# Kernel tuning notes

Hardware: AMD Instinct MI355X
Metric: run time of the kernel (lower is better)

## Reference

```python
import jax, jax.numpy as jnp
import numpy as np

D_K = 24
ALPHA = 0.1
N_HEADS = 6
D_MODEL = 144
LN_EPS = 1e-5


def setup_inputs() -> dict:
    key = jax.random.key(0)
    ks = jax.random.split(key, 8)
    B, S = 8, 2048
    Q = jax.random.normal(ks[0], (B, S, D_MODEL), dtype=jnp.float32)
    K = jax.random.normal(ks[1], (B, N_HEADS, S, D_K), dtype=jnp.float32)
    V = jax.random.normal(ks[2], (B, N_HEADS, S, D_K), dtype=jnp.float32)
    attn_mask = jax.random.randint(ks[3], (B, S, S), 0, 2).astype(bool)
    Wq_w = jax.random.normal(ks[4], (D_MODEL, D_MODEL), dtype=jnp.float32) * 0.05
    Wq_b = jnp.zeros((D_MODEL,), dtype=jnp.float32)
    lin_w = jax.random.normal(ks[5], (D_MODEL, D_MODEL), dtype=jnp.float32) * 0.05
    lin_b = jnp.zeros((D_MODEL,), dtype=jnp.float32)
    ln_g = jnp.ones((D_MODEL,), dtype=jnp.float32)
    ln_b = jnp.zeros((D_MODEL,), dtype=jnp.float32)
    return {"Q": Q, "K": K, "V": V, "attn_mask": attn_mask,
            "Wq_w": Wq_w, "Wq_b": Wq_b, "lin_w": lin_w, "lin_b": lin_b,
            "ln_g": ln_g, "ln_b": ln_b}


def reference(Q, K, V, attn_mask, Wq_w, Wq_b, lin_w, lin_b, ln_g, ln_b):
    B, S, _ = Q.shape
    residual = Q
    # W_Q projection then head split: [B,S,D] -> [B,H,S,d_k]
    q = (Q @ Wq_w.T + Wq_b).reshape(B, S, N_HEADS, D_K).transpose(0, 2, 1, 3)
    # scores [B,H,S,Sk]; custom tanh activation instead of softmax
    scores = jnp.einsum('bhqd,bhkd->bhqk', q, K) / np.sqrt(D_K).astype(np.float32)
    attn = jnp.tanh(ALPHA * scores)
    # NOTE: original calls attn.masked_fill(...) non-inplace and drops the
    # result, so attn_mask has no effect. Faithfully ignored here.
    context = jnp.einsum('bhqk,bhkd->bhqd', attn, V)
    context = context.transpose(0, 2, 1, 3).reshape(B, S, N_HEADS * D_K)
    output = context @ lin_w.T + lin_b
    x = output + residual
    mu = jnp.mean(x, axis=-1, keepdims=True)
    var = jnp.var(x, axis=-1, keepdims=True)
    return (x - mu) / jnp.sqrt(var + LN_EPS) * ln_g + ln_b
```

## Files before the change

kernel.cpp:

```cpp
#include <hip/hip_runtime.h>
#include <hip/hip_bf16.h>

#define B_  8
#define S_  2048
#define H_  6
#define DK_ 24
#define DM_ 144

#define TK0  2.0412414523193153e-02f
#define TK1 -2.8350575726379381e-06f
#define TK2  4.7250959543965635e-10f

typedef __bf16 bf16x8 __attribute__((ext_vector_type(8)));
typedef __bf16 bf16x2 __attribute__((ext_vector_type(2)));
typedef float  f32x4  __attribute__((ext_vector_type(4)));
typedef float  f32x2  __attribute__((ext_vector_type(2)));

#define MFMA_ __builtin_amdgcn_mfma_f32_16x16x32_bf16

__device__ __forceinline__ unsigned short f2bf(float f) {
    return __builtin_bit_cast(unsigned short, (__bf16)f);
}
__device__ __forceinline__ uint pack2(float a, float b) {
    bf16x2 v; v[0] = (__bf16)a; v[1] = (__bf16)b;
    return __builtin_bit_cast(uint, v);
}
__device__ __forceinline__ uint tanh2_pack(float a, float b) {
    f32x2 c; c[0] = a; c[1] = b;
    f32x2 t = c * c;
    f32x2 u = t * TK2 + TK1;
    u = t * u + TK0;
    f32x2 r = c * u;
    return pack2(r[0], r[1]);
}

__device__ __forceinline__ void swap32(uint &x, uint &y) {
    auto r = __builtin_amdgcn_permlane32_swap(x, y, false, false);
    x = r[0]; y = r[1];
}
__device__ __forceinline__ void swap16(uint &x, uint &y, bool hi16) {
#if __has_builtin(__builtin_amdgcn_permlane16_swap)
    (void)hi16;
    auto r = __builtin_amdgcn_permlane16_swap(x, y, false, false);
    x = r[0]; y = r[1];
#else
    uint xs = __builtin_amdgcn_ds_swizzle(x, 0x401F);
    uint ys = __builtin_amdgcn_ds_swizzle(y, 0x401F);
    uint nx = hi16 ? ys : x;
    uint ny = hi16 ? y : xs;
    x = nx; y = ny;
#endif
}

__global__ __launch_bounds__(256)
void prep_kernel(const float* __restrict__ K, const float* __restrict__ V,
                 const float* __restrict__ Wq, const float* __restrict__ Wqb,
                 const float* __restrict__ Wl, const float* __restrict__ lb,
                 ushort* __restrict__ Ktt, ushort* __restrict__ Vtt,
                 ushort* __restrict__ Whq, ushort* __restrict__ Wlp) {
    __shared__ float sv[64 * 25];
    const int t = threadIdx.x;
    const int bid = blockIdx.x;
    if (bid >= 1536) {
        int i = (bid - 1536) * 256 + t;
        if (i < 30720) {
            int h = i / 5120, rem = i % 5120;
            int d = rem / 160, c = rem % 160;
            float v = 0.f;
            if (d < DK_) {
                if (c < DM_)       v = Wq[(h * DK_ + d) * DM_ + c];
                else if (c == DM_) v = Wqb[h * DK_ + d];
            }
            Whq[i] = f2bf(v);
        } else if (i < 53760) {
            int j = i - 30720;
            int r = j / 160, c = j % 160;
            float v = (c < DM_) ? Wl[r * DM_ + c] : (c == DM_ ? lb[r] : 0.f);
            Wlp[j] = f2bf(v);
        }
        return;
    }
    const int kt = bid & 31, h = (bid >> 5) % H_, b = bid / (32 * H_);
    const int bh = b * H_ + h;
    const size_t tile = (size_t)(bh * 32 + kt);
    const float4* Ks = (const float4*)(K + ((size_t)bh * S_ + kt * 64) * DK_);
    ushort* Ko = Ktt + tile * 2048;
    for (int idx = t; idx < 384; idx += 256) {
        int r = idx / 6, c4 = (idx % 6) * 4;
        float4 v = Ks[idx];
        ushort4 u; u.x = f2bf(v.x); u.y = f2bf(v.y); u.z = f2bf(v.z); u.w = f2bf(v.w);
        *(ushort4*)&Ko[r * 32 + c4] = u;
    }
    if (t < 64) { uint4 z = {0u,0u,0u,0u}; *(uint4*)&Ko[t * 32 + 24] = z; }
    const float4* Vs = (const float4*)(V + ((size_t)bh * S_ + kt * 64) * DK_);
    for (int idx = t; idx < 384; idx += 256) {
        int r = idx / 6, c4 = (idx % 6) * 4;
        *(float4*)&sv[r * 25 + c4] = Vs[idx];
    }
    __syncthreads();
    int d = t >> 3, s8 = (t & 7) * 8;
    uint4 o = {0u,0u,0u,0u};
    if (d < DK_) {
        o.x = pack2(sv[(s8 + 0) * 25 + d], sv[(s8 + 1) * 25 + d]);
        o.y = pack2(sv[(s8 + 2) * 25 + d], sv[(s8 + 3) * 25 + d]);
        o.z = pack2(sv[(s8 + 4) * 25 + d], sv[(s8 + 5) * 25 + d]);
        o.w = pack2(sv[(s8 + 6) * 25 + d], sv[(s8 + 7) * 25 + d]);
    }
    ((uint4*)Vtt)[tile * 256 + t] = o;
}

__global__ __launch_bounds__(512, 6)
void attn_kernel(const float* __restrict__ Q, const ushort* __restrict__ Whq,
                 const ushort* __restrict__ Ktt, const ushort* __restrict__ Vtt,
                 ushort* __restrict__ Cb) {
    __shared__ __attribute__((aligned(16))) char smem[38912];
    ushort* s_k  = (ushort*)smem;
    ushort* s_vt = (ushort*)(smem + 20480);
    ushort* s_q  = (ushort*)smem;
    float*  s_ctx = (float*)smem;

    const int t = threadIdx.x;
    const int w = t >> 6, n16 = t & 15, g = (t >> 4) & 3;
    const bool hi16 = (t & 16) != 0;
    const int qp = blockIdx.x, h = blockIdx.y, b = blockIdx.z;
    const int bh = b * H_ + h;
    const int row0 = qp * 128;

    const uint4* Kb4 = (const uint4*)Ktt + (size_t)bh * 8192;
    const uint4* Vb4 = (const uint4*)Vtt + (size_t)bh * 8192;

    const int t2 = t & 255;
    const bool isK = (t < 256);
    const int stoff = isK ? ((t2 >> 2) * 40 + (t2 & 3) * 8)
                          : ((t2 >> 3) * 72 + (t2 & 7) * 8);
    uint4 sreg0 = isK ? Kb4[t2] : Vb4[t2];
    uint4 sreg1 = isK ? Kb4[256 + t2] : Vb4[256 + t2];

    const f32x4 zf = {0.f, 0.f, 0.f, 0.f};
    const uint4* Wh4 = (const uint4*)Whq + h * 640;
    {
        const float* Qr = Q + (size_t)(b * S_ + row0 + w * 16 + n16) * DM_;
        f32x4 qa0 = zf, qa1 = zf;
#pragma unroll
        for (int ks = 0; ks < 5; ++ks) {
            bf16x8 av;
            if (ks < 4 || g < 2) {
                float4 f0 = *(const float4*)&Qr[ks * 32 + g * 8];
                float4 f1 = *(const float4*)&Qr[ks * 32 + g * 8 + 4];
                uint4 u;
                u.x = pack2(f0.x, f0.y); u.y = pack2(f0.z, f0.w);
                u.z = pack2(f1.x, f1.y); u.w = pack2(f1.z, f1.w);
                av = __builtin_bit_cast(bf16x8, u);
            } else {
                uint4 u = {0u, 0u, 0u, 0u};
                if (g == 2) u.x = 0x00003F80u;
                av = __builtin_bit_cast(bf16x8, u);
            }
            bf16x8 bv0 = __builtin_bit_cast(bf16x8, Wh4[n16 * 20 + ks * 4 + g]);
            bf16x8 bv1 = __builtin_bit_cast(bf16x8, Wh4[(16 + n16) * 20 + ks * 4 + g]);
            qa0 = MFMA_(av, bv0, qa0, 0, 0, 0);
            qa1 = MFMA_(av, bv1, qa1, 0, 0, 0);
        }
#pragma unroll
        for (int reg = 0; reg < 4; ++reg) {
            int r = (w * 16 + g * 4 + reg) * 40;
            s_q[r + n16]      = f2bf(qa0[reg]);
            s_q[r + 16 + n16] = f2bf(qa1[reg]);
        }
    }
    const bf16x8 qf = *(const bf16x8*)&s_q[(w * 16 + n16) * 40 + g * 8];
    __syncthreads();

    const int aoff = n16 * 40 + g * 8;
    const int voff = n16 * 72 + g * 8;
    f32x4 acc0 = zf, acc1 = zf;

    for (int c = 0; c < 16; ++c) {
        ushort* kc = s_k + (c & 1) * 5120;
        ushort* vc = s_vt + (c & 1) * 4608;
        if (isK) { *(uint4*)&kc[stoff] = sreg0; *(uint4*)&kc[2560 + stoff] = sreg1; }
        else     { *(uint4*)&vc[stoff] = sreg0; *(uint4*)&vc[2304 + stoff] = sreg1; }
        __syncthreads();
        {
            int nt = ((2 * c + 2) & 31) * 256;
            sreg0 = isK ? Kb4[nt + t2] : Vb4[nt + t2];
            sreg1 = isK ? Kb4[nt + 256 + t2] : Vb4[nt + 256 + t2];
        }
#pragma unroll
        for (int p = 0; p < 2; ++p) {
            const ushort* kp = kc + p * 2560;
            const ushort* vp = vc + p * 2304;
            bf16x8 a0 = *(const bf16x8*)&kp[aoff];
            bf16x8 a1 = *(const bf16x8*)&kp[640 + aoff];
            bf16x8 a2 = *(const bf16x8*)&kp[1280 + aoff];
            bf16x8 a3 = *(const bf16x8*)&kp[1920 + aoff];
            __builtin_amdgcn_s_setprio(1);
            f32x4 c0 = MFMA_(a0, qf, zf, 0, 0, 0);
            f32x4 c1 = MFMA_(a1, qf, zf, 0, 0, 0);
            f32x4 c2 = MFMA_(a2, qf, zf, 0, 0, 0);
            f32x4 c3 = MFMA_(a3, qf, zf, 0, 0, 0);
            __builtin_amdgcn_s_setprio(0);
            uint W0p0 = tanh2_pack(c0[0], c0[1]);
            uint W0p1 = tanh2_pack(c0[2], c0[3]);
            uint W1p0 = tanh2_pack(c1[0], c1[1]);
            uint W1p1 = tanh2_pack(c1[2], c1[3]);
            uint W2p0 = tanh2_pack(c2[0], c2[1]);
            uint W2p1 = tanh2_pack(c2[2], c2[3]);
            uint W3p0 = tanh2_pack(c3[0], c3[1]);
            uint W3p1 = tanh2_pack(c3[2], c3[3]);
            swap32(W0p0, W1p0);
            swap32(W2p0, W3p0);
            swap32(W0p1, W1p1);
            swap32(W2p1, W3p1);
            swap16(W0p0, W1p0, hi16);
            swap16(W2p0, W3p0, hi16);
            swap16(W0p1, W1p1, hi16);
            swap16(W2p1, W3p1, hi16);
            uint4 ap0u, ap1u;
            ap0u.x = W0p0; ap0u.y = W0p1; ap0u.z = W1p0; ap0u.w = W1p1;
            ap1u.x = W2p0; ap1u.y = W2p1; ap1u.z = W3p0; ap1u.w = W3p1;
            bf16x8 ap0 = __builtin_bit_cast(bf16x8, ap0u);
            bf16x8 ap1 = __builtin_bit_cast(bf16x8, ap1u);
            bf16x8 vb00 = *(const bf16x8*)&vp[voff];
            bf16x8 vb01 = *(const bf16x8*)&vp[voff + 32];
            bf16x8 vb10 = *(const bf16x8*)&vp[1152 + voff];
            bf16x8 vb11 = *(const bf16x8*)&vp[1152 + voff + 32];
            __builtin_amdgcn_s_setprio(1);
            acc0 = MFMA_(ap0, vb00, acc0, 0, 0, 0);
            acc0 = MFMA_(ap1, vb01, acc0, 0, 0, 0);
            acc1 = MFMA_(ap0, vb10, acc1, 0, 0, 0);
            acc1 = MFMA_(ap1, vb11, acc1, 0, 0, 0);
            __builtin_amdgcn_s_setprio(0);
        }
    }

    __syncthreads();
#pragma unroll
    for (int reg = 0; reg < 4; ++reg) {
        int row = w * 16 + g * 4 + reg;
        s_ctx[row * 28 + n16] = acc0[reg];
        if (n16 < 8) s_ctx[row * 28 + 16 + n16] = acc1[reg];
    }
    __syncthreads();
    if (t < 384) {
        int r = t / 3, c = t % 3;
        const float* src = &s_ctx[r * 28 + c * 8];
        uint4 u;
        u.x = pack2(src[0], src[1]); u.y = pack2(src[2], src[3]);
        u.z = pack2(src[4], src[5]); u.w = pack2(src[6], src[7]);
        *(uint4*)&Cb[(size_t)(b * S_ + row0 + r) * 160 + h * 24 + c * 8] = u;
    }
}

__global__ __launch_bounds__(1024)
void outln_kernel(const float* __restrict__ Qres, const ushort* __restrict__ Wlp,
                  const ushort* __restrict__ Cb,
                  const float* __restrict__ lg, const float* __restrict__ lbeta,
                  float* __restrict__ io) {
    __shared__ __attribute__((aligned(16))) ushort s_a[64 * 168];
    __shared__ __attribute__((aligned(16))) ushort s_w[144 * 168];
    __shared__ float s_red[4][2][64];
    const int t = threadIdx.x;
    const int w = t >> 6, n16 = t & 15, g = (t >> 4) & 3;
    const int wq = w & 3, jg = w >> 2;
    const int nt_base = (jg == 0) ? 0 : (1 + 2 * jg);
    const int nt_cnt  = (jg == 0) ? 3 : 2;
    const int row0 = blockIdx.x * 64;

    const ushort* Cr = Cb + (size_t)row0 * 160;
    for (int idx = t; idx < 1152; idx += 1024) {
        int r = idx / 18, c8 = (idx % 18) * 8;
        *(uint4*)&s_a[r * 168 + c8] = *(const uint4*)&Cr[r * 160 + c8];
    }
    if (t < 64) {
        uint4 pad = {0x00003F80u, 0u, 0u, 0u};
        uint4 z4  = {0u, 0u, 0u, 0u};
        *(uint4*)&s_a[t * 168 + 144] = pad;
        *(uint4*)&s_a[t * 168 + 152] = z4;
    }
    for (int idx = t; idx < 2880; idx += 1024) {
        int r = idx / 20, c8 = (idx % 20) * 8;
        *(uint4*)&s_w[r * 168 + c8] = *(const uint4*)&Wlp[r * 160 + c8];
    }
    __syncthreads();

    f32x4 acc[3];
#pragma unroll
    for (int j = 0; j < 3; ++j) acc[j] = (f32x4){0.f, 0.f, 0.f, 0.f};
#pragma unroll
    for (int ks = 0; ks < 5; ++ks) {
        bf16x8 av = *(const bf16x8*)&s_a[(wq * 16 + n16) * 168 + ks * 32 + g * 8];
        for (int j = 0; j < nt_cnt; ++j) {
            bf16x8 bv = *(const bf16x8*)&s_w[((nt_base + j) * 16 + n16) * 168 + ks * 32 + g * 8];
            acc[j] = MFMA_(av, bv, acc[j], 0, 0, 0);
        }
    }
    float vals[3][4], s1[4] = {0, 0, 0, 0}, s2[4] = {0, 0, 0, 0};
    for (int j = 0; j < nt_cnt; ++j) {
        int d = (nt_base + j) * 16 + n16;
#pragma unroll
        for (int reg = 0; reg < 4; ++reg) {
            int row = row0 + wq * 16 + g * 4 + reg;
            float v = acc[j][reg] + Qres[(size_t)row * DM_ + d];
            vals[j][reg] = v;
            s1[reg] += v; s2[reg] = fmaf(v, v, s2[reg]);
        }
    }
#pragma unroll
    for (int off = 1; off < 16; off <<= 1) {
#pragma unroll
        for (int reg = 0; reg < 4; ++reg) {
            s1[reg] += __shfl_xor(s1[reg], off);
            s2[reg] += __shfl_xor(s2[reg], off);
        }
    }
    if (n16 == 0) {
#pragma unroll
        for (int reg = 0; reg < 4; ++reg) {
            int rr = wq * 16 + g * 4 + reg;
            s_red[jg][0][rr] = s1[reg];
            s_red[jg][1][rr] = s2[reg];
        }
    }
    __syncthreads();
    float mu[4], rs[4];
#pragma unroll
    for (int reg = 0; reg < 4; ++reg) {
        int rr = wq * 16 + g * 4 + reg;
        float S1 = s_red[0][0][rr] + s_red[1][0][rr] + s_red[2][0][rr] + s_red[3][0][rr];
        float S2 = s_red[0][1][rr] + s_red[1][1][rr] + s_red[2][1][rr] + s_red[3][1][rr];
        float m = S1 * (1.f / 144.f);
        mu[reg] = m;
        rs[reg] = rsqrtf(S2 * (1.f / 144.f) - m * m + 1e-5f);
    }
    for (int j = 0; j < nt_cnt; ++j) {
        int d = (nt_base + j) * 16 + n16;
        float gv = lg[d], bv = lbeta[d];
#pragma unroll
        for (int reg = 0; reg < 4; ++reg) {
            int row = row0 + wq * 16 + g * 4 + reg;
            io[(size_t)row * DM_ + d] = (vals[j][reg] - mu[reg]) * rs[reg] * gv + bv;
        }
    }
}

extern "C" void kernel_launch(void* const* d_in, const int* in_sizes, int n_in,
                              void* d_out, int out_size, void* d_ws, size_t ws_size,
                              hipStream_t stream) {
    const float* Q     = (const float*)d_in[0];
    const float* K     = (const float*)d_in[1];
    const float* V     = (const float*)d_in[2];
    const float* Wq_w  = (const float*)d_in[4];
    const float* Wq_b  = (const float*)d_in[5];
    const float* lin_w = (const float*)d_in[6];
    const float* lin_b = (const float*)d_in[7];
    const float* ln_g  = (const float*)d_in[8];
    const float* ln_b  = (const float*)d_in[9];
    float* out = (float*)d_out;

    ushort* Ktt = (ushort*)d_ws;
    ushort* Vtt = (ushort*)((char*)d_ws + 6291456);
    ushort* Whq = (ushort*)((char*)d_ws + 12582912);
    ushort* Wlp = (ushort*)((char*)d_ws + 12644352);
    ushort* Cb  = (ushort*)((char*)d_ws + 12690432);

    prep_kernel<<<1746, 256, 0, stream>>>(K, V, Wq_w, Wq_b, lin_w, lin_b,
                                          Ktt, Vtt, Whq, Wlp);
    attn_kernel<<<dim3(S_ / 128, H_, B_), 512, 0, stream>>>(Q, Whq, Ktt, Vtt, Cb);
    outln_kernel<<<(B_ * S_) / 64, 1024, 0, stream>>>(Q, Wlp, Cb, ln_g, ln_b, out);
}
```

Measured before the change: 253.2 us.

## Fuse K and weight bf16 conversion into consumer kernels, drop prep pass

K is no longer pre-converted to a padded bf16 layout; the attention kernel loads fp32 K and packs it to bf16 while staging tiles into shared memory. The Wq and linear weights are likewise converted on the fly inside the attention and output kernels, so the prep kernel only transposes V. This removes a global write-and-reread of K and the weight prep blocks, in exchange for more bytes per K tile load (fp32), conversion work repeated across every block, and redundant weight reads.

```diff
diff --git a/kernel.cpp b/kernel.cpp
--- a/kernel.cpp
+++ b/kernel.cpp
@@ -32,6 +32,12 @@
     u = t * u + TK0;
     f32x2 r = c * u;
     return pack2(r[0], r[1]);
+}
+__device__ __forceinline__ uint4 pack8(const float4& fa, const float4& fb) {
+    uint4 u;
+    u.x = pack2(fa.x, fa.y); u.y = pack2(fa.z, fa.w);
+    u.z = pack2(fb.x, fb.y); u.w = pack2(fb.z, fb.w);
+    return u;
 }
 
 __device__ __forceinline__ void swap32(uint &x, uint &y) {
@@ -53,45 +59,12 @@
 }
 
 __global__ __launch_bounds__(256)
-void prep_kernel(const float* __restrict__ K, const float* __restrict__ V,
-                 const float* __restrict__ Wq, const float* __restrict__ Wqb,
-                 const float* __restrict__ Wl, const float* __restrict__ lb,
-                 ushort* __restrict__ Ktt, ushort* __restrict__ Vtt,
-                 ushort* __restrict__ Whq, ushort* __restrict__ Wlp) {
+void prep_v_kernel(const float* __restrict__ V, ushort* __restrict__ Vtt) {
     __shared__ float sv[64 * 25];
     const int t = threadIdx.x;
     const int bid = blockIdx.x;
-    if (bid >= 1536) {
-        int i = (bid - 1536) * 256 + t;
-        if (i < 30720) {
-            int h = i / 5120, rem = i % 5120;
-            int d = rem / 160, c = rem % 160;
-            float v = 0.f;
-            if (d < DK_) {
-                if (c < DM_)       v = Wq[(h * DK_ + d) * DM_ + c];
-                else if (c == DM_) v = Wqb[h * DK_ + d];
-            }
-            Whq[i] = f2bf(v);
-        } else if (i < 53760) {
-            int j = i - 30720;
-            int r = j / 160, c = j % 160;
-            float v = (c < DM_) ? Wl[r * DM_ + c] : (c == DM_ ? lb[r] : 0.f);
-            Wlp[j] = f2bf(v);
-        }
-        return;
-    }
-    const int kt = bid & 31, h = (bid >> 5) % H_, b = bid / (32 * H_);
-    const int bh = b * H_ + h;
+    const int kt = bid & 31, bh = bid >> 5;
     const size_t tile = (size_t)(bh * 32 + kt);
-    const float4* Ks = (const float4*)(K + ((size_t)bh * S_ + kt * 64) * DK_);
-    ushort* Ko = Ktt + tile * 2048;
-    for (int idx = t; idx < 384; idx += 256) {
-        int r = idx / 6, c4 = (idx % 6) * 4;
-        float4 v = Ks[idx];
-        ushort4 u; u.x = f2bf(v.x); u.y = f2bf(v.y); u.z = f2bf(v.z); u.w = f2bf(v.w);
-        *(ushort4*)&Ko[r * 32 + c4] = u;
-    }
-    if (t < 64) { uint4 z = {0u,0u,0u,0u}; *(uint4*)&Ko[t * 32 + 24] = z; }
     const float4* Vs = (const float4*)(V + ((size_t)bh * S_ + kt * 64) * DK_);
     for (int idx = t; idx < 384; idx += 256) {
         int r = idx / 6, c4 = (idx % 6) * 4;
@@ -110,9 +83,9 @@
 }
 
 __global__ __launch_bounds__(512, 6)
-void attn_kernel(const float* __restrict__ Q, const ushort* __restrict__ Whq,
-                 const ushort* __restrict__ Ktt, const ushort* __restrict__ Vtt,
-                 ushort* __restrict__ Cb) {
+void attn_kernel(const float* __restrict__ Q, const float* __restrict__ K,
+                 const float* __restrict__ Wq, const float* __restrict__ Wqb,
+                 const ushort* __restrict__ Vtt, ushort* __restrict__ Cb) {
     __shared__ __attribute__((aligned(16))) char smem[38912];
     ushort* s_k  = (ushort*)smem;
     ushort* s_vt = (ushort*)(smem + 20480);
@@ -126,20 +99,33 @@
     const int bh = b * H_ + h;
     const int row0 = qp * 128;
 
-    const uint4* Kb4 = (const uint4*)Ktt + (size_t)bh * 8192;
     const uint4* Vb4 = (const uint4*)Vtt + (size_t)bh * 8192;
+    const float* Kf  = K + (size_t)bh * S_ * DK_;
 
     const int t2 = t & 255;
     const bool isK = (t < 256);
-    const int stoff = isK ? ((t2 >> 2) * 40 + (t2 & 3) * 8)
+    const int krow = t2 >> 2, kcq = t2 & 3;
+    const bool kreal = isK && (kcq < 3);
+    const int stoff = isK ? (krow * 40 + kcq * 8)
                           : ((t2 >> 3) * 72 + (t2 & 7) * 8);
-    uint4 sreg0 = isK ? Kb4[t2] : Vb4[t2];
-    uint4 sreg1 = isK ? Kb4[256 + t2] : Vb4[256 + t2];
+    float4 kf0a, kf0b, kf1a, kf1b;
+    uint4 sv0, sv1;
+    if (isK) {
+        if (kreal) {
+            const float* p0 = &Kf[(size_t)krow * DK_ + kcq * 8];
+            kf0a = *(const float4*)p0; kf0b = *(const float4*)(p0 + 4);
+            const float* p1 = &Kf[(size_t)(64 + krow) * DK_ + kcq * 8];
+            kf1a = *(const float4*)p1; kf1b = *(const float4*)(p1 + 4);
+        }
+    } else {
+        sv0 = Vb4[t2]; sv1 = Vb4[256 + t2];
+    }
 
     const f32x4 zf = {0.f, 0.f, 0.f, 0.f};
-    const uint4* Wh4 = (const uint4*)Whq + h * 640;
     {
         const float* Qr = Q + (size_t)(b * S_ + row0 + w * 16 + n16) * DM_;
+        const float* Wqh  = Wq + (size_t)h * DK_ * DM_;
+        const float* Wqbh = Wqb + h * DK_;
         f32x4 qa0 = zf, qa1 = zf;
 #pragma unroll
         for (int ks = 0; ks < 5; ++ks) {
@@ -147,17 +133,36 @@
             if (ks < 4 || g < 2) {
                 float4 f0 = *(const float4*)&Qr[ks * 32 + g * 8];
                 float4 f1 = *(const float4*)&Qr[ks * 32 + g * 8 + 4];
-                uint4 u;
-                u.x = pack2(f0.x, f0.y); u.y = pack2(f0.z, f0.w);
-                u.z = pack2(f1.x, f1.y); u.w = pack2(f1.z, f1.w);
-                av = __builtin_bit_cast(bf16x8, u);
+                av = __builtin_bit_cast(bf16x8, pack8(f0, f1));
             } else {
                 uint4 u = {0u, 0u, 0u, 0u};
                 if (g == 2) u.x = 0x00003F80u;
                 av = __builtin_bit_cast(bf16x8, u);
             }
-            bf16x8 bv0 = __builtin_bit_cast(bf16x8, Wh4[n16 * 20 + ks * 4 + g]);
-            bf16x8 bv1 = __builtin_bit_cast(bf16x8, Wh4[(16 + n16) * 20 + ks * 4 + g]);
+            bf16x8 bv0, bv1;
+            {
+                uint4 u = {0u, 0u, 0u, 0u};
+                if (ks < 4 || g < 2) {
+                    const float* p = &Wqh[n16 * DM_ + ks * 32 + g * 8];
+                    u = pack8(*(const float4*)p, *(const float4*)(p + 4));
+                } else if (g == 2) {
+                    u.x = pack2(Wqbh[n16], 0.f);
+                }
+                bv0 = __builtin_bit_cast(bf16x8, u);
+            }
+            {
+                uint4 u = {0u, 0u, 0u, 0u};
+                if (n16 < 8) {
+                    int d = 16 + n16;
+                    if (ks < 4 || g < 2) {
+                        const float* p = &Wqh[d * DM_ + ks * 32 + g * 8];
+                        u = pack8(*(const float4*)p, *(const float4*)(p + 4));
+                    } else if (g == 2) {
+                        u.x = pack2(Wqbh[d], 0.f);
+                    }
+                }
+                bv1 = __builtin_bit_cast(bf16x8, u);
+            }
             qa0 = MFMA_(av, bv0, qa0, 0, 0, 0);
             qa1 = MFMA_(av, bv1, qa1, 0, 0, 0);
         }
@@ -178,13 +183,29 @@
     for (int c = 0; c < 16; ++c) {
         ushort* kc = s_k + (c & 1) * 5120;
         ushort* vc = s_vt + (c & 1) * 4608;
-        if (isK) { *(uint4*)&kc[stoff] = sreg0; *(uint4*)&kc[2560 + stoff] = sreg1; }
-        else     { *(uint4*)&vc[stoff] = sreg0; *(uint4*)&vc[2304 + stoff] = sreg1; }
+        if (isK) {
+            uint4 u0 = {0u,0u,0u,0u}, u1 = {0u,0u,0u,0u};
+            if (kreal) { u0 = pack8(kf0a, kf0b); u1 = pack8(kf1a, kf1b); }
+            *(uint4*)&kc[stoff] = u0;
+            *(uint4*)&kc[2560 + stoff] = u1;
+        } else {
+            *(uint4*)&vc[stoff] = sv0;
+            *(uint4*)&vc[2304 + stoff] = sv1;
+        }
         __syncthreads();
         {
-            int nt = ((2 * c + 2) & 31) * 256;
-            sreg0 = isK ? Kb4[nt + t2] : Vb4[nt + t2];
-            sreg1 = isK ? Kb4[nt + 256 + t2] : Vb4[nt + 256 + t2];
+            int nt = (2 * c + 2) & 31;
+            if (isK) {
+                if (kreal) {
+                    const float* p0 = &Kf[(size_t)(nt * 64 + krow) * DK_ + kcq * 8];
+                    kf0a = *(const float4*)p0; kf0b = *(const float4*)(p0 + 4);
+                    const float* p1 = &Kf[(size_t)((nt + 1) * 64 + krow) * DK_ + kcq * 8];
+                    kf1a = *(const float4*)p1; kf1b = *(const float4*)(p1 + 4);
+                }
+            } else {
+                sv0 = Vb4[nt * 256 + t2];
+                sv1 = Vb4[nt * 256 + 256 + t2];
+            }
         }
 #pragma unroll
         for (int p = 0; p < 2; ++p) {
@@ -253,8 +274,8 @@
 }
 
 __global__ __launch_bounds__(1024)
-void outln_kernel(const float* __restrict__ Qres, const ushort* __restrict__ Wlp,
-                  const ushort* __restrict__ Cb,
+void outln_kernel(const float* __restrict__ Qres, const float* __restrict__ Wl,
+                  const float* __restrict__ lb, const ushort* __restrict__ Cb,
                   const float* __restrict__ lg, const float* __restrict__ lbeta,
                   float* __restrict__ io) {
     __shared__ __attribute__((aligned(16))) ushort s_a[64 * 168];
@@ -280,7 +301,14 @@
     }
     for (int idx = t; idx < 2880; idx += 1024) {
         int r = idx / 20, c8 = (idx % 20) * 8;
-        *(uint4*)&s_w[r * 168 + c8] = *(const uint4*)&Wlp[r * 160 + c8];
+        uint4 u = {0u, 0u, 0u, 0u};
+        if (c8 < DM_) {
+            const float* p = &Wl[r * DM_ + c8];
+            u = pack8(*(const float4*)p, *(const float4*)(p + 4));
+        } else if (c8 == DM_) {
+            u.x = pack2(lb[r], 0.f);
+        }
+        *(uint4*)&s_w[r * 168 + c8] = u;
     }
     __syncthreads();
 
@@ -358,14 +386,10 @@
     const float* ln_b  = (const float*)d_in[9];
     float* out = (float*)d_out;
 
-    ushort* Ktt = (ushort*)d_ws;
-    ushort* Vtt = (ushort*)((char*)d_ws + 6291456);
-    ushort* Whq = (ushort*)((char*)d_ws + 12582912);
-    ushort* Wlp = (ushort*)((char*)d_ws + 12644352);
-    ushort* Cb  = (ushort*)((char*)d_ws + 12690432);
-
-    prep_kernel<<<1746, 256, 0, stream>>>(K, V, Wq_w, Wq_b, lin_w, lin_b,
-                                          Ktt, Vtt, Whq, Wlp);
-    attn_kernel<<<dim3(S_ / 128, H_, B_), 512, 0, stream>>>(Q, Whq, Ktt, Vtt, Cb);
-    outln_kernel<<<(B_ * S_) / 64, 1024, 0, stream>>>(Q, Wlp, Cb, ln_g, ln_b, out);
-}
+    ushort* Vtt = (ushort*)d_ws;
+    ushort* Cb  = (ushort*)((char*)d_ws + 6291456);
+
+    prep_v_kernel<<<1536, 256, 0, stream>>>(V, Vtt);
+    attn_kernel<<<dim3(S_ / 128, H_, B_), 512, 0, stream>>>(Q, K, Wq_w, Wq_b, Vtt, Cb);
+    outln_kernel<<<(B_ * S_) / 64, 1024, 0, stream>>>(Q, lin_w, lin_b, Cb, ln_g, ln_b, out);
+}
```

Measured after the change: 255.0 us, median of 2. About the same (+0.7%).
